# Kernel tuning notes

Measured on AMD Instinct MI355X. Metric: run time of the kernel, lower is better.

Reference implementation:

```python
import jax, jax.numpy as jnp
import numpy as np

DIN = 4096
DOUT = 12288
NUM_GATES = DOUT // 3
OFFSET = 1
BS = 4096
Z = 1.0

# fixed 3x5 combine matrix from the module
M = jnp.array([[1., 0., 0., 0., 0.],
               [0., 0., 1., 1., -1.],
               [0., 1., 0., -1., 1.]], dtype=jnp.float32)


def _make_connections():
    g = np.arange(NUM_GATES, dtype=np.int64)
    starts = (g * 3 + OFFSET) % DIN
    conn = (starts[:, None] + np.arange(3, dtype=np.int64)[None, :]) % DIN
    return jnp.asarray(conn, dtype=jnp.int32)


def setup_inputs() -> dict:
    key = jax.random.key(0)
    kx, kw = jax.random.split(key)
    x = jax.random.normal(kx, (BS, DIN), dtype=jnp.float32)
    wgts = jax.random.normal(kw, (NUM_GATES, 3, 4), dtype=jnp.float32)
    connections = _make_connections()
    return {"x": x, "wgts": wgts, "connections": connections}


def reference(x, wgts, connections):
    bs = x.shape[0]
    # gather 3 inputs per gate: [bs, G, 3]
    gathered = x[:, connections]
    # append constant z -> [bs, G, 4]
    zcol = jnp.full((bs, NUM_GATES, 1), Z, dtype=x.dtype)
    inp = jnp.concatenate([gathered, zcol], axis=-1)
    # softmax-weighted small matmul (training path): [G,3,4] x [bs,G,4] -> [bs,G,3]
    wp = jax.nn.softmax(wgts, axis=-1)
    s = jnp.einsum('gik,bgk->bgi', wp, inp)
    # elementwise products -> [bs, G, 5]
    v4 = s[..., 0] * s[..., 1]
    v5 = s[..., 0] * s[..., 2]
    feats = jnp.concatenate([s, v4[..., None], v5[..., None]], axis=-1)
    # fixed 3x5 combine: [bs, G, 3]
    signals = jnp.einsum('rk,bgk->bgr', M, feats)
    # strided slice ::3 on last dim (size 3) keeps only index 0 -> [bs, G]
    out = signals[:, :, ::3].reshape(bs, -1)
    return out
```

## Files before the change

### kernel.cpp

```cpp
#include <hip/hip_runtime.h>

#define DIN  4096
#define NG   4096
#define BS   4096
#define ROWS_PER_BLOCK 16
#define GATES_PER_THREAD 4
#define BLOCK_THREADS 256

typedef float v4f __attribute__((ext_vector_type(4)));

__global__ __launch_bounds__(BLOCK_THREADS) void fredkin_s0_kernel(
    const float* __restrict__ x,
    const float* __restrict__ wgts,
    float* __restrict__ out)
{
    const int tg = blockIdx.x * BLOCK_THREADS + threadIdx.x;
    const int g0 = tg * GATES_PER_THREAD;

    float4 w[GATES_PER_THREAD];
#pragma unroll
    for (int j = 0; j < GATES_PER_THREAD; ++j) {
        float4 r = *reinterpret_cast<const float4*>(wgts + (size_t)(g0 + j) * 12);
        float m  = fmaxf(fmaxf(r.x, r.y), fmaxf(r.z, r.w));
        float e0 = __expf(r.x - m);
        float e1 = __expf(r.y - m);
        float e2 = __expf(r.z - m);
        float e3 = __expf(r.w - m);
        float inv = 1.0f / (e0 + e1 + e2 + e3);
        w[j] = make_float4(e0 * inv, e1 * inv, e2 * inv, e3 * inv);
    }

    const int base = (tg * 12) & (DIN - 1);
    const int i0 = base;
    const int i1 = (base + 4)  & (DIN - 1);
    const int i2 = (base + 8)  & (DIN - 1);
    const int i3 = (base + 12) & (DIN - 1);

    const int brow = blockIdx.y * ROWS_PER_BLOCK;
    const float* xr   = x   + (size_t)brow * DIN;
    float*       orow = out + (size_t)brow * NG + g0;

#pragma unroll 2
    for (int r = 0; r < ROWS_PER_BLOCK; ++r) {
        float4 f0 = *reinterpret_cast<const float4*>(xr + i0);
        float4 f1 = *reinterpret_cast<const float4*>(xr + i1);
        float4 f2 = *reinterpret_cast<const float4*>(xr + i2);
        float  e12 = xr[i3];

        v4f o;
        o.x = fmaf(w[0].x, f0.y, fmaf(w[0].y, f0.z, fmaf(w[0].z, f0.w, w[0].w)));
        o.y = fmaf(w[1].x, f1.x, fmaf(w[1].y, f1.y, fmaf(w[1].z, f1.z, w[1].w)));
        o.z = fmaf(w[2].x, f1.w, fmaf(w[2].y, f2.x, fmaf(w[2].z, f2.y, w[2].w)));
        o.w = fmaf(w[3].x, f2.z, fmaf(w[3].y, f2.w, fmaf(w[3].z, e12, w[3].w)));

        __builtin_nontemporal_store(o, reinterpret_cast<v4f*>(orow));

        xr   += DIN;
        orow += NG;
    }
}

extern "C" void kernel_launch(void* const* d_in, const int* in_sizes, int n_in,
                              void* d_out, int out_size, void* d_ws, size_t ws_size,
                              hipStream_t stream) {
    const float* x    = (const float*)d_in[0];
    const float* wgts = (const float*)d_in[1];
    float* out = (float*)d_out;

    dim3 grid(NG / (BLOCK_THREADS * GATES_PER_THREAD),
              BS / ROWS_PER_BLOCK);
    fredkin_s0_kernel<<<grid, dim3(BLOCK_THREADS), 0, stream>>>(x, wgts, out);
}
```

Measured before the change: 133.4 us.

## Stage x rows in double-buffered LDS so each element is loaded once

Each block now handles whole rows with 1024 threads. Every thread loads one coalesced float4 of the current x row into a double-buffered shared-memory row, with a small halo for wraparound, and prefetches the next row into a register. The overlapping 3-wide gate gathers then read from LDS instead of global memory, so global traffic for x drops to a single read per element. The cost is a __syncthreads per row, possible LDS bank conflicts from the stride-12 reads, and large 1024-thread blocks that may limit occupancy.

```diff
diff --git a/kernel.cpp b/kernel.cpp
--- a/kernel.cpp
+++ b/kernel.cpp
@@ -3,23 +3,25 @@
 #define DIN  4096
 #define NG   4096
 #define BS   4096
-#define ROWS_PER_BLOCK 16
-#define GATES_PER_THREAD 4
-#define BLOCK_THREADS 256
+#define RPB  8
+#define BT   1024
+#define WROW 4112
 
 typedef float v4f __attribute__((ext_vector_type(4)));
 
-__global__ __launch_bounds__(BLOCK_THREADS) void fredkin_s0_kernel(
+__global__ __launch_bounds__(BT) void fredkin_s0_dbuf(
     const float* __restrict__ x,
     const float* __restrict__ wgts,
     float* __restrict__ out)
 {
-    const int tg = blockIdx.x * BLOCK_THREADS + threadIdx.x;
-    const int g0 = tg * GATES_PER_THREAD;
+    __shared__ float xs[2][WROW];
 
-    float4 w[GATES_PER_THREAD];
+    const int tid = threadIdx.x;
+    const int g0  = 4 * tid;
+
+    float4 w[4];
 #pragma unroll
-    for (int j = 0; j < GATES_PER_THREAD; ++j) {
+    for (int j = 0; j < 4; ++j) {
         float4 r = *reinterpret_cast<const float4*>(wgts + (size_t)(g0 + j) * 12);
         float m  = fmaxf(fmaxf(r.x, r.y), fmaxf(r.z, r.w));
         float e0 = __expf(r.x - m);
@@ -30,22 +32,29 @@
         w[j] = make_float4(e0 * inv, e1 * inv, e2 * inv, e3 * inv);
     }
 
-    const int base = (tg * 12) & (DIN - 1);
-    const int i0 = base;
-    const int i1 = (base + 4)  & (DIN - 1);
-    const int i2 = (base + 8)  & (DIN - 1);
-    const int i3 = (base + 12) & (DIN - 1);
+    const int lb = (12 * tid) & (DIN - 1);
 
-    const int brow = blockIdx.y * ROWS_PER_BLOCK;
-    const float* xr   = x   + (size_t)brow * DIN;
+    const int brow = blockIdx.x * RPB;
+    const float* xr   = x   + (size_t)brow * DIN + 4 * tid;
     float*       orow = out + (size_t)brow * NG + g0;
 
-#pragma unroll 2
-    for (int r = 0; r < ROWS_PER_BLOCK; ++r) {
-        float4 f0 = *reinterpret_cast<const float4*>(xr + i0);
-        float4 f1 = *reinterpret_cast<const float4*>(xr + i1);
-        float4 f2 = *reinterpret_cast<const float4*>(xr + i2);
-        float  e12 = xr[i3];
+    float4 v = *reinterpret_cast<const float4*>(xr);
+
+    for (int r = 0; r < RPB; ++r) {
+        float* buf = xs[r & 1];
+        *reinterpret_cast<float4*>(&buf[4 * tid]) = v;
+        if (tid < 4)
+            *reinterpret_cast<float4*>(&buf[DIN + 4 * tid]) = v;
+
+        if (r + 1 < RPB)
+            v = *reinterpret_cast<const float4*>(xr + DIN);
+
+        __syncthreads();
+
+        float4 f0 = *reinterpret_cast<const float4*>(&buf[lb]);
+        float4 f1 = *reinterpret_cast<const float4*>(&buf[lb + 4]);
+        float4 f2 = *reinterpret_cast<const float4*>(&buf[lb + 8]);
+        float  e12 = buf[lb + 12];
 
         v4f o;
         o.x = fmaf(w[0].x, f0.y, fmaf(w[0].y, f0.z, fmaf(w[0].z, f0.w, w[0].w)));
@@ -67,7 +76,5 @@
     const float* wgts = (const float*)d_in[1];
     float* out = (float*)d_out;
 
-    dim3 grid(NG / (BLOCK_THREADS * GATES_PER_THREAD),
-              BS / ROWS_PER_BLOCK);
-    fredkin_s0_kernel<<<grid, dim3(BLOCK_THREADS), 0, stream>>>(x, wgts, out);
+    fredkin_s0_dbuf<<<dim3(BS / RPB), dim3(BT), 0, stream>>>(x, wgts, out);
 }
```

Result: faster. 124.4 us (-6.7%).
